# Kernel tuning notes

Measured on AMD Instinct MI355X. Metric: run time of the kernel, lower is better.

The kernel has to match this reference:

```python
import jax, jax.numpy as jnp
import numpy as np

D_MODEL = 1024

def setup_inputs() -> dict:
    key = jax.random.key(0)
    ks = jax.random.split(key, 7)
    x = jax.random.normal(ks[0], (4, 2048, D_MODEL), dtype=jnp.float32)
    s = 1.0 / np.sqrt(D_MODEL)
    Wq = jax.random.uniform(ks[1], (D_MODEL, D_MODEL), jnp.float32, -s, s)
    bq = jax.random.uniform(ks[2], (D_MODEL,), jnp.float32, -s, s)
    Wk = jax.random.uniform(ks[3], (D_MODEL, D_MODEL), jnp.float32, -s, s)
    bk = jax.random.uniform(ks[4], (D_MODEL,), jnp.float32, -s, s)
    Wv = jax.random.uniform(ks[5], (D_MODEL, D_MODEL), jnp.float32, -s, s)
    bv = jax.random.uniform(ks[6], (D_MODEL,), jnp.float32, -s, s)
    return {"x": x, "Wq": Wq, "bq": bq, "Wk": Wk, "bk": bk, "Wv": Wv, "bv": bv}

def reference(x, Wq, bq, Wk, bk, Wv, bv):
    # single-head self-attention: q,k,v are [B, S, D]
    q = x @ Wq + bq
    k = x @ Wk + bk
    v = x @ Wv + bv
    scale = 1.0 / jnp.sqrt(jnp.asarray(D_MODEL, x.dtype))
    scores = jnp.einsum('bsd,btd->bst', q, k) * scale  # [B, S, S]
    attn = jax.nn.softmax(scores, axis=-1)
    return jnp.einsum('bst,btd->bsd', attn, v)
```

## Files before the change

kernel.cpp:

```cpp
#include <hip/hip_runtime.h>
#include <hip/hip_bf16.h>
#include <stdint.h>


typedef __attribute__((ext_vector_type(8))) short short8;
typedef __attribute__((ext_vector_type(4))) float f32x4;

__device__ __forceinline__ unsigned short f2bf(float f) {
  union { float f; uint32_t u; } c; c.f = f;
  uint32_t u = c.u;
  u += 0x7FFFu + ((u >> 16) & 1u);
  return (unsigned short)(u >> 16);
}

__device__ __forceinline__ void gl16(const void* g, void* l) {
  __builtin_amdgcn_global_load_lds(
      (const __attribute__((address_space(1))) unsigned int*)g,
      (__attribute__((address_space(3))) unsigned int*)l, 16, 0, 0);
}

#define FENCE() asm volatile("" ::: "memory")
#define BARRIER() do { FENCE(); __builtin_amdgcn_s_barrier(); FENCE(); } while (0)
#define VMWAIT(n) asm volatile("s_waitcnt vmcnt(" #n ")" ::: "memory")

__global__ __launch_bounds__(512, 2) void k_qkv(
    const short* __restrict__ A, const short* __restrict__ B,
    short* __restrict__ Cb, short* __restrict__ vT,
    const float* __restrict__ b0, const float* __restrict__ b1,
    const float* __restrict__ b2)
{
  __shared__ short lds[65536];

  const int b = blockIdx.x;
  const int xcd = b & 7, r = b >> 3;
  const int tm = xcd * 4 + r / 12;
  const int zn = r % 12;
  const int z = zn >> 2, tn = zn & 3;

  const int tid = threadIdx.x;
  const int lane = tid & 63;
  const int wid = tid >> 6;
  const int fr = lane & 15, quad = lane >> 4, frk = fr & 7;
  const int wm = wid >> 2, wn = wid & 3;

  const long tileM = (long)tm * 256;
  const long tileN = (long)tn * 256;
  const short* Az = A;
  const short* Bz = B + (long)z * 1048576L;

  const int srow = tid >> 3;
  const int sslot = (tid & 7) ^ (srow & 7);
  const short* gA = Az + (tileM + srow) * 1024 + sslot * 8;
  const short* gB = Bz + (tileN + srow) * 1024 + sslot * 8;

  const int aBase = wm << 13;
  const int bBase = 16384 + (wn << 12);
  const int o0 = ((quad ^ frk) << 3) + (fr << 6);
  const int o1 = (((quad + 4) ^ frk) << 3) + (fr << 6);

  f32x4 acc[8][4] = {};

  auto stageA = [&](int tt) {
    const short* s = gA + tt * 64;
    short* d = &lds[(tt & 1) << 15];
    gl16(s,          d + (tid << 3));
    gl16(s + 65536,  d + 4096 + (tid << 3));
    gl16(s + 131072, d + 8192 + (tid << 3));
    gl16(s + 196608, d + 12288 + (tid << 3));
  };
  auto stageBh = [&](int tt, int h) {
    const short* s = gB + tt * 64 + h * 131072;
    short* d = &lds[((tt & 1) << 15) + 16384 + (h << 13)];
    gl16(s,         d + (tid << 3));
    gl16(s + 65536, d + 4096 + (tid << 3));
  };

  stageA(0); stageBh(0, 0); stageBh(0, 1); stageA(1);
  VMWAIT(4);
  BARRIER();

#pragma unroll 1
  for (int t = 0; t < 16; ++t) {
    const int bb = (t & 1) << 15;
    short8 af0[4][2], af1[4][2], bf0[2][2], bf1[2][2];

#pragma unroll
    for (int i = 0; i < 4; ++i) {
      af0[i][0] = *(const short8*)&lds[bb + aBase + (i << 10) + o0];
      af0[i][1] = *(const short8*)&lds[bb + aBase + (i << 10) + o1];
    }
#pragma unroll
    for (int j = 0; j < 2; ++j) {
      bf0[j][0] = *(const short8*)&lds[bb + bBase + (j << 10) + o0];
      bf0[j][1] = *(const short8*)&lds[bb + bBase + (j << 10) + o1];
    }
    if (t + 1 < 16) stageBh(t + 1, 0);
    BARRIER();
    __builtin_amdgcn_s_setprio(1);
#pragma unroll
    for (int i = 0; i < 4; ++i)
#pragma unroll
      for (int j = 0; j < 2; ++j) {
        acc[i][j] = __builtin_amdgcn_mfma_f32_16x16x32_bf16(af0[i][0], bf0[j][0], acc[i][j], 0, 0, 0);
        acc[i][j] = __builtin_amdgcn_mfma_f32_16x16x32_bf16(af0[i][1], bf0[j][1], acc[i][j], 0, 0, 0);
      }
    __builtin_amdgcn_s_setprio(0);
    BARRIER();

#pragma unroll
    for (int i = 0; i < 4; ++i) {
      af1[i][0] = *(const short8*)&lds[bb + aBase + ((i + 4) << 10) + o0];
      af1[i][1] = *(const short8*)&lds[bb + aBase + ((i + 4) << 10) + o1];
    }
    if (t + 1 < 16) stageBh(t + 1, 1);
    BARRIER();
    __builtin_amdgcn_s_setprio(1);
#pragma unroll
    for (int i = 0; i < 4; ++i)
#pragma unroll
      for (int j = 0; j < 2; ++j) {
        acc[i + 4][j] = __builtin_amdgcn_mfma_f32_16x16x32_bf16(af1[i][0], bf0[j][0], acc[i + 4][j], 0, 0, 0);
        acc[i + 4][j] = __builtin_amdgcn_mfma_f32_16x16x32_bf16(af1[i][1], bf0[j][1], acc[i + 4][j], 0, 0, 0);
      }
    __builtin_amdgcn_s_setprio(0);
    BARRIER();

#pragma unroll
    for (int j = 0; j < 2; ++j) {
      bf1[j][0] = *(const short8*)&lds[bb + bBase + ((j + 2) << 10) + o0];
      bf1[j][1] = *(const short8*)&lds[bb + bBase + ((j + 2) << 10) + o1];
    }
    BARRIER();
    __builtin_amdgcn_s_setprio(1);
#pragma unroll
    for (int i = 0; i < 4; ++i)
#pragma unroll
      for (int j = 0; j < 2; ++j) {
        acc[i + 4][j + 2] = __builtin_amdgcn_mfma_f32_16x16x32_bf16(af1[i][0], bf1[j][0], acc[i + 4][j + 2], 0, 0, 0);
        acc[i + 4][j + 2] = __builtin_amdgcn_mfma_f32_16x16x32_bf16(af1[i][1], bf1[j][1], acc[i + 4][j + 2], 0, 0, 0);
      }
    __builtin_amdgcn_s_setprio(0);
    BARRIER();

    if (t + 2 < 16) stageA(t + 2);
    BARRIER();
    __builtin_amdgcn_s_setprio(1);
#pragma unroll
    for (int i = 0; i < 4; ++i)
#pragma unroll
      for (int j = 0; j < 2; ++j) {
        acc[i][j + 2] = __builtin_amdgcn_mfma_f32_16x16x32_bf16(af0[i][0], bf1[j][0], acc[i][j + 2], 0, 0, 0);
        acc[i][j + 2] = __builtin_amdgcn_mfma_f32_16x16x32_bf16(af0[i][1], bf1[j][1], acc[i][j + 2], 0, 0, 0);
      }
    __builtin_amdgcn_s_setprio(0);
    if (t < 14) { VMWAIT(4); } else { VMWAIT(0); }
    BARRIER();
  }

  __syncthreads();
  short* scr = &lds[wid * 4608];
  if (z == 2) {
    const int gb = tm >> 3;
#pragma unroll
    for (int pass = 0; pass < 2; ++pass) {
#pragma unroll
      for (int j = 0; j < 4; ++j) {
        const float bv = b2[tileN + wn * 64 + j * 16 + fr];
#pragma unroll
        for (int i = 0; i < 4; ++i)
#pragma unroll
          for (int rr = 0; rr < 4; ++rr)
            scr[(j * 16 + fr) * 72 + i * 16 + quad * 4 + rr] =
                (short)f2bf(acc[pass * 4 + i][j][rr] + bv);
      }
      const long t0 = (long)(tm & 7) * 256 + wm * 128 + pass * 64;
#pragma unroll
      for (int c = 0; c < 8; ++c) {
        const int rr = c * 8 + (lane >> 3);
        const int cc = (lane & 7) * 8;
        short8 v = *(const short8*)&scr[rr * 72 + cc];
        const long gd = tileN + wn * 64 + rr;
        *(short8*)(vT + ((long)gb << 21) + gd * 2048 + t0 + cc) = v;
      }
      if (pass == 0) __syncthreads();
    }
  } else {
    short* C = Cb + (long)z * 8388608L;
    const float* bias = (z == 0) ? b0 : b1;
#pragma unroll
    for (int pass = 0; pass < 2; ++pass) {
#pragma unroll
      for (int j = 0; j < 4; ++j) {
        const float bv = bias[tileN + wn * 64 + j * 16 + fr];
#pragma unroll
        for (int i = 0; i < 4; ++i)
#pragma unroll
          for (int rr = 0; rr < 4; ++rr)
            scr[(i * 16 + quad * 4 + rr) * 72 + j * 16 + fr] =
                (short)f2bf(acc[pass * 4 + i][j][rr] + bv);
      }
#pragma unroll
      for (int c = 0; c < 8; ++c) {
        const int row = c * 8 + (lane >> 3);
        const int col = (lane & 7) * 8;
        short8 v = *(const short8*)&scr[row * 72 + col];
        *(short8*)(C + (tileM + wm * 128 + pass * 64 + row) * 1024 +
                   tileN + wn * 64 + col) = v;
      }
      if (pass == 0) __syncthreads();
    }
  }
}

__global__ __launch_bounds__(512, 2) void k_score(
    const short* __restrict__ A, const short* __restrict__ B,
    short* __restrict__ Pp, float scale, float* __restrict__ rowsum)
{
  __shared__ short lds[65536];

  const int b = blockIdx.x;
  const int xcd = b & 7, jb = b >> 3;
  const int p = xcd * 4 + (jb >> 3);
  const int tn = jb & 7;
  const int z = p >> 3, tm = p & 7;

  const int tid = threadIdx.x;
  const int lane = tid & 63;
  const int wid = tid >> 6;
  const int fr = lane & 15, quad = lane >> 4;
  const int wm = wid >> 2, wn = wid & 3;

  const long tileM = (long)tm * 256;
  const long tileN = (long)tn * 256;
  const short* Az = A + (long)z * 2097152L;
  const short* Bz = B + (long)z * 2097152L;

  const int srow = tid >> 3;
  const int sslot = (tid & 7) ^ (srow & 7);
  const short* gA = Az + (tileM + srow) * 1024 + sslot * 8;
  const short* gB = Bz + (tileN + srow) * 1024 + sslot * 8;

  const int frk = fr & 7;
  const int aBase = wm << 13;
  const int bRow  = 16384 + ((wn >> 1) << 13) + ((wn & 1) << 12);
  const int o0 = ((quad ^ frk) << 3) + (fr << 6);
  const int o1 = (((quad + 4) ^ frk) << 3) + (fr << 6);

  f32x4 acc[8][4] = {};

  auto stageA = [&](int tt) {
    const short* s = gA + tt * 64;
    short* d = &lds[(tt & 1) << 15];
    gl16(s,          d + (tid << 3));
    gl16(s + 65536,  d + 4096 + (tid << 3));
    gl16(s + 131072, d + 8192 + (tid << 3));
    gl16(s + 196608, d + 12288 + (tid << 3));
  };
  auto stageBh = [&](int tt, int h) {
    const short* s = gB + tt * 64 + h * 131072;
    short* d = &lds[((tt & 1) << 15) + 16384 + (h << 13)];
    gl16(s,         d + (tid << 3));
    gl16(s + 65536, d + 4096 + (tid << 3));
  };

  stageA(0); stageBh(0, 0); stageBh(0, 1); stageA(1);
  VMWAIT(4);
  BARRIER();

#pragma unroll 1
  for (int t = 0; t < 16; ++t) {
    const int bb = (t & 1) << 15;
    short8 af0[4][2], af1[4][2], bf0[2][2], bf1[2][2];

#pragma unroll
    for (int i = 0; i < 4; ++i) {
      af0[i][0] = *(const short8*)&lds[bb + aBase + (i << 10) + o0];
      af0[i][1] = *(const short8*)&lds[bb + aBase + (i << 10) + o1];
    }
#pragma unroll
    for (int j = 0; j < 2; ++j) {
      bf0[j][0] = *(const short8*)&lds[bb + bRow + (j << 10) + o0];
      bf0[j][1] = *(const short8*)&lds[bb + bRow + (j << 10) + o1];
    }
    if (t + 1 < 16) stageBh(t + 1, 0);
    BARRIER();
    __builtin_amdgcn_s_setprio(1);
#pragma unroll
    for (int i = 0; i < 4; ++i)
#pragma unroll
      for (int j = 0; j < 2; ++j) {
        acc[i][j] = __builtin_amdgcn_mfma_f32_16x16x32_bf16(af0[i][0], bf0[j][0], acc[i][j], 0, 0, 0);
        acc[i][j] = __builtin_amdgcn_mfma_f32_16x16x32_bf16(af0[i][1], bf0[j][1], acc[i][j], 0, 0, 0);
      }
    __builtin_amdgcn_s_setprio(0);
    BARRIER();

#pragma unroll
    for (int i = 0; i < 4; ++i) {
      af1[i][0] = *(const short8*)&lds[bb + aBase + ((i + 4) << 10) + o0];
      af1[i][1] = *(const short8*)&lds[bb + aBase + ((i + 4) << 10) + o1];
    }
    if (t + 1 < 16) stageBh(t + 1, 1);
    BARRIER();
    __builtin_amdgcn_s_setprio(1);
#pragma unroll
    for (int i = 0; i < 4; ++i)
#pragma unroll
      for (int j = 0; j < 2; ++j) {
        acc[i + 4][j] = __builtin_amdgcn_mfma_f32_16x16x32_bf16(af1[i][0], bf0[j][0], acc[i + 4][j], 0, 0, 0);
        acc[i + 4][j] = __builtin_amdgcn_mfma_f32_16x16x32_bf16(af1[i][1], bf0[j][1], acc[i + 4][j], 0, 0, 0);
      }
    __builtin_amdgcn_s_setprio(0);
    BARRIER();

#pragma unroll
    for (int j = 0; j < 2; ++j) {
      bf1[j][0] = *(const short8*)&lds[bb + bRow + ((j + 2) << 10) + o0];
      bf1[j][1] = *(const short8*)&lds[bb + bRow + ((j + 2) << 10) + o1];
    }
    BARRIER();
    __builtin_amdgcn_s_setprio(1);
#pragma unroll
    for (int i = 0; i < 4; ++i)
#pragma unroll
      for (int j = 0; j < 2; ++j) {
        acc[i + 4][j + 2] = __builtin_amdgcn_mfma_f32_16x16x32_bf16(af1[i][0], bf1[j][0], acc[i + 4][j + 2], 0, 0, 0);
        acc[i + 4][j + 2] = __builtin_amdgcn_mfma_f32_16x16x32_bf16(af1[i][1], bf1[j][1], acc[i + 4][j + 2], 0, 0, 0);
      }
    __builtin_amdgcn_s_setprio(0);
    BARRIER();

    if (t + 2 < 16) stageA(t + 2);
    BARRIER();
    __builtin_amdgcn_s_setprio(1);
#pragma unroll
    for (int i = 0; i < 4; ++i)
#pragma unroll
      for (int j = 0; j < 2; ++j) {
        acc[i][j + 2] = __builtin_amdgcn_mfma_f32_16x16x32_bf16(af0[i][0], bf1[j][0], acc[i][j + 2], 0, 0, 0);
        acc[i][j + 2] = __builtin_amdgcn_mfma_f32_16x16x32_bf16(af0[i][1], bf1[j][1], acc[i][j + 2], 0, 0, 0);
      }
    __builtin_amdgcn_s_setprio(0);
    if (t < 14) { VMWAIT(4); } else { VMWAIT(0); }
    BARRIER();
  }

#pragma unroll
  for (int i = 0; i < 8; ++i)
#pragma unroll
    for (int j = 0; j < 4; ++j)
#pragma unroll
      for (int r = 0; r < 4; ++r)
        acc[i][j][r] = exp2f(acc[i][j][r] * scale);

  float* rsz = rowsum + (long)z * 2048 + tileM + wm * 128;
#pragma unroll
  for (int i = 0; i < 8; ++i)
#pragma unroll
    for (int r = 0; r < 4; ++r) {
      float s = acc[i][0][r] + acc[i][1][r] + acc[i][2][r] + acc[i][3][r];
      s += __shfl_xor(s, 1);
      s += __shfl_xor(s, 2);
      s += __shfl_xor(s, 4);
      s += __shfl_xor(s, 8);
      if (fr == 0) atomicAdd(&rsz[i * 16 + quad * 4 + r], s);
    }

  __syncthreads();
  short* C = Pp + (long)z * 4194304L;
  short* scr = &lds[wid * 4608];
#pragma unroll
  for (int pass = 0; pass < 2; ++pass) {
#pragma unroll
    for (int j = 0; j < 4; ++j)
#pragma unroll
      for (int i = 0; i < 4; ++i)
#pragma unroll
        for (int r = 0; r < 4; ++r)
          scr[(i * 16 + quad * 4 + r) * 72 + j * 16 + fr] =
              (short)f2bf(acc[pass * 4 + i][j][r]);
#pragma unroll
    for (int c = 0; c < 8; ++c) {
      const int row = c * 8 + (lane >> 3);
      const int col = (lane & 7) * 8;
      short8 v = *(const short8*)&scr[row * 72 + col];
      *(short8*)(C + (tileM + wm * 128 + pass * 64 + row) * 2048 +
                 tileN + wn * 64 + col) = v;
    }
  }
}

__global__ __launch_bounds__(256) void k_pv(
    const short* __restrict__ A, const short* __restrict__ B,
    float* __restrict__ Cf, float* __restrict__ rowsum)
{
  const int b = blockIdx.x;
  const int s = b & 7, r0_ = b >> 3;
  const int z = r0_ >> 4;
  const int mem = r0_ & 15;
  const int tm = (s >> 1) * 4 + (mem >> 2);
  const int tn = (s & 1) * 4 + (mem & 3);

  __shared__ short lds[18432];

  const int tid  = threadIdx.x;
  const int lane = tid & 63;
  const int wid  = tid >> 6;
  const long tileM = (long)tm * 128;
  const long tileN = (long)tn * 128;
  const short* Az = A + (long)z * 4194304L;
  const short* Bz = B + (long)z * 2097152L;

  const int c0 = tid, c1 = 256 + tid;
  const short* gA0 = Az + (tileM + (c0 >> 2)) * 2048 + (c0 & 3) * 8;
  const short* gA1 = Az + (tileM + (c1 >> 2)) * 2048 + (c1 & 3) * 8;
  const short* gB0 = Bz + (tileN + (c0 >> 2)) * 2048 + (c0 & 3) * 8;
  const short* gB1 = Bz + (tileN + (c1 >> 2)) * 2048 + (c1 & 3) * 8;

  const int fr = lane & 15, quad = lane >> 4;
  const int waveM = (wid >> 1) * 64, waveN = (wid & 1) * 64;

  f32x4 acc[4][4] = {};

  {
    short* base = lds;
    gl16(gA0, base + c0 * 8);
    gl16(gA1, base + c1 * 8);
    gl16(gB0, base + 4096 + c0 * 8);
    gl16(gB1, base + 4096 + c1 * 8);
  }

  for (int t = 0; t < 64; ++t) {
    __syncthreads();
    if (t + 1 < 64) {
      const int kt = (t + 1) << 5;
      short* base = lds + ((t + 1) & 1) * 8192;
      gl16(gA0 + kt, base + c0 * 8);
      gl16(gA1 + kt, base + c1 * 8);
      gl16(gB0 + kt, base + 4096 + c0 * 8);
      gl16(gB1 + kt, base + 4096 + c1 * 8);
    }
    const short* sA = lds + (t & 1) * 8192;
    const short* sB = sA + 4096;
    short8 af[4], bf[4];
#pragma unroll
    for (int i = 0; i < 4; ++i)
      af[i] = *(const short8*)&sA[(waveM + i * 16 + fr) * 32 + quad * 8];
#pragma unroll
    for (int j = 0; j < 4; ++j)
      bf[j] = *(const short8*)&sB[(waveN + j * 16 + fr) * 32 + quad * 8];
#pragma unroll
    for (int i = 0; i < 4; ++i)
#pragma unroll
      for (int j = 0; j < 4; ++j)
        acc[i][j] = __builtin_amdgcn_mfma_f32_16x16x32_bf16(af[i], bf[j],
                                                            acc[i][j], 0, 0, 0);
  }

  float* C = Cf + (long)z * 2097152L;
#pragma unroll
  for (int i = 0; i < 4; ++i)
#pragma unroll
    for (int r = 0; r < 4; ++r) {
      const long gr = tileM + waveM + i * 16 + quad * 4 + r;
      const float rinv = 1.0f / rowsum[(long)z * 2048 + gr];
#pragma unroll
      for (int j = 0; j < 4; ++j)
        C[gr * 1024 + tileN + waveN + j * 16 + fr] = acc[i][j][r] * rinv;
    }
}

__global__ __launch_bounds__(256) void k_prep(
    const float4* __restrict__ x, ushort4* __restrict__ xb,
    const float* __restrict__ Wq, const float* __restrict__ Wk,
    const float* __restrict__ Wv, short* __restrict__ WT,
    float* __restrict__ rs)
{
  __shared__ short tile[32][33];
  const int b = blockIdx.x;
  if (b < 8192) {
    const long i = (long)b * 256 + threadIdx.x;
    float4 v = x[i];
    ushort4 o;
    o.x = f2bf(v.x); o.y = f2bf(v.y); o.z = f2bf(v.z); o.w = f2bf(v.w);
    xb[i] = o;
  } else if (b < 11264) {
    const int idx = b - 8192;
    const int z = idx >> 10, rem = idx & 1023;
    const float* W = (z == 0) ? Wq : ((z == 1) ? Wk : Wv);
    short* d = WT + (long)z * 1024 * 1024;
    const int n0 = (rem & 31) * 32, d0 = (rem >> 5) * 32;
    const int tx = threadIdx.x & 31, ty = threadIdx.x >> 5;
#pragma unroll
    for (int p = 0; p < 4; ++p)
      tile[ty + p * 8][tx] = (short)f2bf(W[(long)(d0 + ty + p * 8) * 1024 + n0 + tx]);
    __syncthreads();
#pragma unroll
    for (int p = 0; p < 4; ++p)
      d[(long)(n0 + ty + p * 8) * 1024 + d0 + tx] = tile[tx][ty + p * 8];
  } else {
#pragma unroll
    for (int p = 0; p < 32; ++p)
      rs[p * 256 + threadIdx.x] = 0.0f;
  }
}

extern "C" void kernel_launch(void* const* d_in, const int* in_sizes, int n_in,
                              void* d_out, int out_size, void* d_ws, size_t ws_size,
                              hipStream_t stream) {
  const float* x  = (const float*)d_in[0];
  const float* Wq = (const float*)d_in[1];
  const float* bq = (const float*)d_in[2];
  const float* Wk = (const float*)d_in[3];
  const float* bk = (const float*)d_in[4];
  const float* Wv = (const float*)d_in[5];
  const float* bv = (const float*)d_in[6];

  char* ws = (char*)d_ws;
  short* xb  = (short*)(ws);
  short* wt  = (short*)(ws + 16777216);
  short* qkv = (short*)(ws + 23068672);
  short* Pp  = (short*)(ws + 73400320);
  float* rs  = (float*)(ws + 106954752);
  short* vT  = qkv + 2L * 8388608;

  k_prep<<<11265, 256, 0, stream>>>((const float4*)x, (ushort4*)xb,
                                    Wq, Wk, Wv, wt, rs);
  k_qkv<<<384, 512, 0, stream>>>(xb, wt, qkv, vT, bq, bk, bv);
  k_score<<<256, 1024 / 2, 0, stream>>>(qkv, qkv + 8388608, Pp,
                                        0.03125f * 1.44269504088896f, rs);
  k_pv<<<512, 256, 0, stream>>>(Pp, vT, (float*)d_out, rs);
}
```

Before: 248.5 us.

## Restructure PV GEMM with 256x128 tiles, 64-wide K, swizzled LDS, split-phase pipeline

Rewrites the attention-times-V kernel so each 512-thread block computes a 256x128 output tile with a 64-deep K step, halving the grid and the number of K iterations. LDS rows are XOR-swizzled to avoid bank conflicts. Each iteration is split into two MFMA phases with the next A/B loads issued in between, using explicit vmcnt waits and s_setprio. Blocks are remapped so each XCD gets contiguous tiles for L2 reuse. In exchange the kernel uses more LDS and registers per block, which may limit occupancy.

```diff
diff --git a/kernel.cpp b/kernel.cpp
--- a/kernel.cpp
+++ b/kernel.cpp
@@ -390,83 +390,120 @@
   }
 }
 
-__global__ __launch_bounds__(256) void k_pv(
+__global__ __launch_bounds__(512, 2) void k_pv(
     const short* __restrict__ A, const short* __restrict__ B,
     float* __restrict__ Cf, float* __restrict__ rowsum)
 {
+  __shared__ short lds[49152];
+
   const int b = blockIdx.x;
-  const int s = b & 7, r0_ = b >> 3;
-  const int z = r0_ >> 4;
-  const int mem = r0_ & 15;
-  const int tm = (s >> 1) * 4 + (mem >> 2);
-  const int tn = (s & 1) * 4 + (mem & 3);
-
-  __shared__ short lds[18432];
-
-  const int tid  = threadIdx.x;
+  const int xcd = b & 7, jb = b >> 3;
+  const int p = xcd * 4 + (jb >> 3);
+  const int tn = jb & 7;
+  const int z = p >> 3, tm = p & 7;
+
+  const int tid = threadIdx.x;
   const int lane = tid & 63;
-  const int wid  = tid >> 6;
-  const long tileM = (long)tm * 128;
+  const int wid = tid >> 6;
+  const int fr = lane & 15, quad = lane >> 4, frk = fr & 7;
+  const int wm = wid >> 1, wn = wid & 1;
+
+  const long tileM = (long)tm * 256;
   const long tileN = (long)tn * 128;
   const short* Az = A + (long)z * 4194304L;
   const short* Bz = B + (long)z * 2097152L;
 
-  const int c0 = tid, c1 = 256 + tid;
-  const short* gA0 = Az + (tileM + (c0 >> 2)) * 2048 + (c0 & 3) * 8;
-  const short* gA1 = Az + (tileM + (c1 >> 2)) * 2048 + (c1 & 3) * 8;
-  const short* gB0 = Bz + (tileN + (c0 >> 2)) * 2048 + (c0 & 3) * 8;
-  const short* gB1 = Bz + (tileN + (c1 >> 2)) * 2048 + (c1 & 3) * 8;
-
-  const int fr = lane & 15, quad = lane >> 4;
-  const int waveM = (wid >> 1) * 64, waveN = (wid & 1) * 64;
+  const int srow = tid >> 3;
+  const int sslot = (tid & 7) ^ (srow & 7);
+  const short* gA = Az + (tileM + srow) * 2048 + sslot * 8;
+  const short* gB = Bz + (tileN + srow) * 2048 + sslot * 8;
+
+  const int aBase = wm << 12;
+  const int bBase = 16384 + (wn << 12);
+  const int o0 = ((quad ^ frk) << 3) + (fr << 6);
+  const int o1 = (((quad + 4) ^ frk) << 3) + (fr << 6);
 
   f32x4 acc[4][4] = {};
 
-  {
-    short* base = lds;
-    gl16(gA0, base + c0 * 8);
-    gl16(gA1, base + c1 * 8);
-    gl16(gB0, base + 4096 + c0 * 8);
-    gl16(gB1, base + 4096 + c1 * 8);
+  auto stageA = [&](int tt) {
+    const short* s = gA + tt * 64;
+    short* d = &lds[(tt & 1) * 24576];
+    gl16(s,          d + (tid << 3));
+    gl16(s + 131072, d + 4096 + (tid << 3));
+    gl16(s + 262144, d + 8192 + (tid << 3));
+    gl16(s + 393216, d + 12288 + (tid << 3));
+  };
+  auto stageB = [&](int tt) {
+    const short* s = gB + tt * 64;
+    short* d = &lds[(tt & 1) * 24576 + 16384];
+    gl16(s,          d + (tid << 3));
+    gl16(s + 131072, d + 4096 + (tid << 3));
+  };
+
+  stageA(0); stageB(0); stageA(1);
+  VMWAIT(4);
+  BARRIER();
+
+#pragma unroll 1
+  for (int t = 0; t < 32; ++t) {
+    const int bb = (t & 1) * 24576;
+    short8 af[4][2], bf0[2][2], bf1[2][2];
+
+#pragma unroll
+    for (int i = 0; i < 4; ++i) {
+      af[i][0] = *(const short8*)&lds[bb + aBase + (i << 10) + o0];
+      af[i][1] = *(const short8*)&lds[bb + aBase + (i << 10) + o1];
+    }
+#pragma unroll
+    for (int j = 0; j < 2; ++j) {
+      bf0[j][0] = *(const short8*)&lds[bb + bBase + (j << 10) + o0];
+      bf0[j][1] = *(const short8*)&lds[bb + bBase + (j << 10) + o1];
+    }
+    if (t + 1 < 32) stageB(t + 1);
+    BARRIER();
+    __builtin_amdgcn_s_setprio(1);
+#pragma unroll
+    for (int i = 0; i < 4; ++i)
+#pragma unroll
+      for (int j = 0; j < 2; ++j) {
+        acc[i][j] = __builtin_amdgcn_mfma_f32_16x16x32_bf16(af[i][0], bf0[j][0], acc[i][j], 0, 0, 0);
+        acc[i][j] = __builtin_amdgcn_mfma_f32_16x16x32_bf16(af[i][1], bf0[j][1], acc[i][j], 0, 0, 0);
+      }
+    __builtin_amdgcn_s_setprio(0);
+    BARRIER();
+
+#pragma unroll
+    for (int j = 0; j < 2; ++j) {
+      bf1[j][0] = *(const short8*)&lds[bb + bBase + ((j + 2) << 10) + o0];
+      bf1[j][1] = *(const short8*)&lds[bb + bBase + ((j + 2) << 10) + o1];
+    }
+    if (t + 2 < 32) stageA(t + 2);
+    BARRIER();
+    __builtin_amdgcn_s_setprio(1);
+#pragma unroll
+    for (int i = 0; i < 4; ++i)
+#pragma unroll
+      for (int j = 0; j < 2; ++j) {
+        acc[i][j + 2] = __builtin_amdgcn_mfma_f32_16x16x32_bf16(af[i][0], bf1[j][0], acc[i][j + 2], 0, 0, 0);
+        acc[i][j + 2] = __builtin_amdgcn_mfma_f32_16x16x32_bf16(af[i][1], bf1[j][1], acc[i][j + 2], 0, 0, 0);
+      }
+    __builtin_amdgcn_s_setprio(0);
+    if (t < 30) { VMWAIT(4); } else { VMWAIT(0); }
+    BARRIER();
   }
 
-  for (int t = 0; t < 64; ++t) {
-    __syncthreads();
-    if (t + 1 < 64) {
-      const int kt = (t + 1) << 5;
-      short* base = lds + ((t + 1) & 1) * 8192;
-      gl16(gA0 + kt, base + c0 * 8);
-      gl16(gA1 + kt, base + c1 * 8);
-      gl16(gB0 + kt, base + 4096 + c0 * 8);
-      gl16(gB1 + kt, base + 4096 + c1 * 8);
-    }
-    const short* sA = lds + (t & 1) * 8192;
-    const short* sB = sA + 4096;
-    short8 af[4], bf[4];
-#pragma unroll
-    for (int i = 0; i < 4; ++i)
-      af[i] = *(const short8*)&sA[(waveM + i * 16 + fr) * 32 + quad * 8];
-#pragma unroll
-    for (int j = 0; j < 4; ++j)
-      bf[j] = *(const short8*)&sB[(waveN + j * 16 + fr) * 32 + quad * 8];
-#pragma unroll
-    for (int i = 0; i < 4; ++i)
+  float* C = Cf + (long)z * 2097152L;
+  const float* rsz = rowsum + (long)z * 2048 + tileM + wm * 64;
+#pragma unroll
+  for (int i = 0; i < 4; ++i)
+#pragma unroll
+    for (int r = 0; r < 4; ++r) {
+      const int lr = i * 16 + quad * 4 + r;
+      const long gr = tileM + wm * 64 + lr;
+      const float rinv = 1.0f / rsz[lr];
 #pragma unroll
       for (int j = 0; j < 4; ++j)
-        acc[i][j] = __builtin_amdgcn_mfma_f32_16x16x32_bf16(af[i], bf[j],
-                                                            acc[i][j], 0, 0, 0);
-  }
-
-  float* C = Cf + (long)z * 2097152L;
-#pragma unroll
-  for (int i = 0; i < 4; ++i)
-#pragma unroll
-    for (int r = 0; r < 4; ++r) {
-      const long gr = tileM + waveM + i * 16 + quad * 4 + r;
-      const float rinv = 1.0f / rowsum[(long)z * 2048 + gr];
-#pragma unroll
-      for (int j = 0; j < 4; ++j)
-        C[gr * 1024 + tileN + waveN + j * 16 + fr] = acc[i][j][r] * rinv;
+        C[gr * 1024 + tileN + wn * 64 + j * 16 + fr] = acc[i][j][r] * rinv;
     }
 }
 
@@ -527,7 +564,7 @@
   k_prep<<<11265, 256, 0, stream>>>((const float4*)x, (ushort4*)xb,
                                     Wq, Wk, Wv, wt, rs);
   k_qkv<<<384, 512, 0, stream>>>(xb, wt, qkv, vT, bq, bk, bv);
-  k_score<<<256, 1024 / 2, 0, stream>>>(qkv, qkv + 8388608, Pp,
-                                        0.03125f * 1.44269504088896f, rs);
-  k_pv<<<512, 256, 0, stream>>>(Pp, vT, (float*)d_out, rs);
-}
+  k_score<<<256, 512, 0, stream>>>(qkv, qkv + 8388608, Pp,
+                                   0.03125f * 1.44269504088896f, rs);
+  k_pv<<<256, 512, 0, stream>>>(Pp, vT, (float*)d_out, rs);
+}
```

New measurement: 241.1 us (median of 2 runs). -3.0%, faster.
